# Kernel tuning notes

Measured on AMD Instinct MI355X. Metric: run time of the kernel, lower is better.

Reference implementation:

```python
import jax, jax.numpy as jnp
import numpy as np

D = 64      # hidden_dim
IN = 32     # input_dim
OUT = 8     # output_dim
WID = 128   # mlp width
B = 128     # batch
N = 16      # seq len
NS = 4      # fixed Tsit5 substeps per observation interval (stand-in for diffrax adaptive solve, max_steps=10)
EPS = 1e-8

# Tsit5 Butcher tableau
_AT = (
    (0.161,),
    (-0.008480655492356989, 0.335480655492357),
    (2.8971530571054935, -6.359448489975075, 4.3622954328695815),
    (5.325864828439257, -11.748883564062828, 7.4955393428898365, -0.09249506636175525),
    (5.86145544294642, -12.92096931784711, 8.159367898576159, -0.071584973281401, -0.028269050394068383),
)
_CT = (0.0, 0.161, 0.327, 0.9, 0.9800255409045097, 1.0)
_BT = (0.09646076681806523, 0.01, 0.4798896504144996, 1.379008574103742, -3.290069515436081, 2.324710524099774)


def _mlp(params, x, act):
    for (Wl, bl) in params[:-1]:
        x = act(Wl @ x + bl)
    Wl, bl = params[-1]
    return Wl @ x + bl


def _attn(h):
    hn = h / (jnp.linalg.norm(h) + EPS)
    return jnp.outer(hn, hn).reshape(-1)


def _field(t, h, a, fp, gp, sf, sg):
    Am = jax.nn.softmax(a.reshape(D, D), axis=-1)
    hp = Am @ h  # h @ softmax(A).T
    inp = jnp.concatenate([hp, t.reshape(1)])
    h_dot = sf * jnp.tanh(_mlp(fp, inp, jax.nn.silu))
    a_dot = sg * jnp.tanh(_mlp(gp, inp, jax.nn.silu))
    return h_dot, a_dot


def setup_inputs() -> dict:
    key = jax.random.key(0)
    ks = jax.random.split(key, 24)
    lin = lambda k, o, i: (jax.random.normal(k, (o, i), jnp.float32) / np.sqrt(i)).astype(jnp.float32)
    dt = jax.random.uniform(ks[0], (B, N), minval=0.05, maxval=0.15)
    ts = jnp.cumsum(dt, axis=1).astype(jnp.float32)
    observations = jax.random.normal(ks[1], (B, N, IN), jnp.float32)
    return {
        "ts": ts, "observations": observations,
        "f_w0": lin(ks[2], WID, D + 1), "f_b0": jnp.zeros((WID,), jnp.float32),
        "f_w1": lin(ks[3], WID, WID),   "f_b1": jnp.zeros((WID,), jnp.float32),
        "f_w2": lin(ks[4], D, WID),     "f_b2": jnp.zeros((D,), jnp.float32),
        "g_w0": lin(ks[5], WID, D + 1), "g_b0": jnp.zeros((WID,), jnp.float32),
        "g_w1": lin(ks[6], WID, WID),   "g_b1": jnp.zeros((WID,), jnp.float32),
        "g_w2": lin(ks[7], D * D, WID), "g_b2": jnp.zeros((D * D,), jnp.float32),
        "f_scale": jnp.array(1.0, jnp.float32), "g_scale": jnp.array(1.0, jnp.float32),
        "rnn_wh": lin(ks[8], D, D), "rnn_wx": lin(ks[9], D, IN), "rnn_b": jnp.zeros((D,), jnp.float32),
        "o_w0": lin(ks[10], WID, D),  "o_b0": jnp.zeros((WID,), jnp.float32),
        "o_w1": lin(ks[11], WID, WID), "o_b1": jnp.zeros((WID,), jnp.float32),
        "o_w2": lin(ks[12], OUT, WID), "o_b2": jnp.zeros((OUT,), jnp.float32),
    }


def reference(ts, observations, f_w0, f_b0, f_w1, f_b1, f_w2, f_b2,
              g_w0, g_b0, g_w1, g_b1, g_w2, g_b2, f_scale, g_scale,
              rnn_wh, rnn_wx, rnn_b, o_w0, o_b0, o_w1, o_b1, o_w2, o_b2):
    fp = ((f_w0, f_b0), (f_w1, f_b1), (f_w2, f_b2))
    gp = ((g_w0, g_b0), (g_w1, g_b1), (g_w2, g_b2))
    op = ((o_w0, o_b0), (o_w1, o_b1), (o_w2, o_b2))

    def single(ts1, obs1):
        h0 = jnp.tanh(rnn_wx @ obs1[0] + rnn_b)  # hidden_linear(zeros) == 0
        a0 = _attn(h0)

        def step(carry, inp):
            h, a = carry
            t0, t1, x = inp
            dt = (t1 - t0) / NS

            def sub(c, i):
                hh, aa = c
                t = t0 + i * dt
                k1h, k1a = _field(t, hh, aa, fp, gp, f_scale, g_scale)
                kh, ka = [k1h], [k1a]
                for s in range(5):
                    hs = hh + dt * sum(_AT[s][j] * kh[j] for j in range(s + 1))
                    as_ = aa + dt * sum(_AT[s][j] * ka[j] for j in range(s + 1))
                    kdh, kda = _field(t + _CT[s + 1] * dt, hs, as_, fp, gp, f_scale, g_scale)
                    kh.append(kdh); ka.append(kda)
                hn = hh + dt * sum(_BT[j] * kh[j] for j in range(6))
                an = aa + dt * sum(_BT[j] * ka[j] for j in range(6))
                return (hn, an), None

            (h_prime, _), _ = jax.lax.scan(sub, (h, a), jnp.arange(NS, dtype=ts1.dtype))
            h_new = jnp.tanh(rnn_wh @ h_prime + rnn_wx @ x + rnn_b)
            return (h_new, _attn(h_new)), None

        (hf, _), _ = jax.lax.scan(step, (h0, a0), (ts1[:-1], ts1[1:], obs1[1:]))
        return _mlp(op, hf, jnp.tanh)

    return jax.vmap(single)(ts, observations)  # (B, OUT), matches batched_call
```

## Files before the change

kernel.cpp:

```cpp
#include <hip/hip_runtime.h>
#include <hip/hip_bf16.h>

#define DH    64
#define INW   32
#define OUTW  8
#define WIDW  128
#define BATCH 128
#define SEQN  16
#define NSUB  4
#define NT    1024

#define OFF_G8   0
#define OFF_L0F  131072
#define OFF_L0G  135296
#define OFF_L1F  139520
#define OFF_L1G  147712
#define OFF_FH   155904
#define OFF_RWH  160000
#define OFF_RWX  164096
#define OFF_OW0  166144
#define OFF_OW1  174336
#define OFF_OW2  190720
#define WS_TOT   191744

typedef float f32x2 __attribute__((ext_vector_type(2)));

__device__ __forceinline__ float fast_tanh(float x){
  float ax = fabsf(x);
  float e  = __expf(-2.f*ax);
  float r  = __fdividef(1.f - e, 1.f + e);
  return copysignf(r, x);
}
__device__ __forceinline__ float fast_silu(float x){
  return x * __fdividef(1.f, 1.f + __expf(-x));
}
__device__ __forceinline__ uint32_t f2bf(float x){
  uint32_t u = __float_as_uint(x);
  return (u + 0x7fffu + ((u >> 16) & 1u)) >> 16;
}
__device__ __forceinline__ uint32_t f32_to_e4m3fn(float x){
  uint32_t u = __float_as_uint(x);
  uint32_t s = (u >> 31) << 7;
  float ax = fabsf(x);
  uint32_t code;
  if (ax < 0.015625f){
    int m = (int)rintf(ax * 512.0f);
    code = s | (uint32_t)m;
  } else {
    uint32_t bb = (u & 0x7FFFFFFFu) + 0x7FFFFu + ((u >> 20) & 1u);
    uint32_t E  = (bb >> 23) - 120u;
    uint32_t mag = (E << 3) | ((bb >> 20) & 7u);
    if (mag > 0x7Eu) mag = 0x7Eu;
    code = s | mag;
  }
  return code;
}

#if __has_builtin(__builtin_amdgcn_cvt_pk_f32_fp8)
__device__ __forceinline__ f32x2 fp8_lo(uint32_t u){ return __builtin_amdgcn_cvt_pk_f32_fp8(u, false); }
__device__ __forceinline__ f32x2 fp8_hi(uint32_t u){ return __builtin_amdgcn_cvt_pk_f32_fp8(u, true); }
#else
__device__ __forceinline__ float fp8_dec1(uint32_t v){
  uint32_t em = v & 0x7Fu;
  float mag;
  if (em >= 8u) mag = __uint_as_float((em + 960u) << 20);
  else          mag = (float)em * 0.001953125f;
  return (v & 0x80u) ? -mag : mag;
}
__device__ __forceinline__ f32x2 fp8_lo(uint32_t u){ f32x2 r; r[0]=fp8_dec1(u&0xFFu); r[1]=fp8_dec1((u>>8)&0xFFu); return r; }
__device__ __forceinline__ f32x2 fp8_hi(uint32_t u){ f32x2 r; r[0]=fp8_dec1((u>>16)&0xFFu); r[1]=fp8_dec1((u>>24)&0xFFu); return r; }
#endif

__device__ __forceinline__ float bflo(uint32_t u){ return __uint_as_float(u << 16); }
__device__ __forceinline__ float bfhi(uint32_t u){ return __uint_as_float(u & 0xFFFF0000u); }

__global__ void prep(const float* __restrict__ fw0, const float* __restrict__ fw1,
                     const float* __restrict__ fw2, const float* __restrict__ gw0,
                     const float* __restrict__ gw1, const float* __restrict__ gw2,
                     const float* __restrict__ rwh, const float* __restrict__ rwx,
                     const float* __restrict__ ow0, const float* __restrict__ ow1,
                     const float* __restrict__ ow2, uint32_t* __restrict__ wsu)
{
  int i = blockIdx.x * 256 + threadIdx.x;
  if (i >= WS_TOT) return;
  float* wsf = (float*)wsu;
  if (i < OFF_L0F){
    int k4 = i >> 12, e = i & 4095;
    uint32_t u = 0;
    #pragma unroll
    for (int j = 0; j < 4; ++j) u |= f32_to_e4m3fn(gw2[e*128 + 4*k4 + j]) << (8*j);
    wsu[i] = u;
  }
  else if (i < OFF_L0G){ int j=i-OFF_L0F; int k2=j>>7, o=j&127; int k0=2*k2;
    uint32_t lo = f2bf(fw0[o*65+k0]); uint32_t hi = (k0+1<65)? f2bf(fw0[o*65+k0+1]) : 0u;
    wsu[i] = lo | (hi<<16); }
  else if (i < OFF_L1F){ int j=i-OFF_L0G; int k2=j>>7, o=j&127; int k0=2*k2;
    uint32_t lo = f2bf(gw0[o*65+k0]); uint32_t hi = (k0+1<65)? f2bf(gw0[o*65+k0+1]) : 0u;
    wsu[i] = lo | (hi<<16); }
  else if (i < OFF_L1G){ int j=i-OFF_L1F; int k2=j>>7, o=j&127;
    wsu[i] = f2bf(fw1[o*128+2*k2]) | (f2bf(fw1[o*128+2*k2+1])<<16); }
  else if (i < OFF_FH){ int j=i-OFF_L1G; int k2=j>>7, o=j&127;
    wsu[i] = f2bf(gw1[o*128+2*k2]) | (f2bf(gw1[o*128+2*k2+1])<<16); }
  else if (i < OFF_RWH){ int j=i-OFF_FH; int k2=j>>6, o=j&63;
    wsu[i] = f2bf(fw2[o*128+2*k2]) | (f2bf(fw2[o*128+2*k2+1])<<16); }
  else if (i < OFF_RWX){ int j=i-OFF_RWH; int k=j>>6, o=j&63; wsf[i] = rwh[o*64+k]; }
  else if (i < OFF_OW0){ int j=i-OFF_RWX; int k=j>>6, o=j&63; wsf[i] = rwx[o*32+k]; }
  else if (i < OFF_OW1){ int j=i-OFF_OW0; int k=j>>7, o=j&127; wsf[i] = ow0[o*64+k]; }
  else if (i < OFF_OW2){ int j=i-OFF_OW1; int k=j>>7, o=j&127; wsf[i] = ow1[o*128+k]; }
  else                 { int j=i-OFF_OW2; int k=j>>3, o=j&7;  wsf[i] = ow2[o*128+k]; }
}

__global__ __launch_bounds__(NT, 4) void ace_main(
    const float* __restrict__ ts,
    const float* __restrict__ obs,
    const float* __restrict__ fb0, const float* __restrict__ fb1, const float* __restrict__ fb2,
    const float* __restrict__ gb0, const float* __restrict__ gb1, const float* __restrict__ gb2,
    const float* __restrict__ fsc, const float* __restrict__ gsc,
    const float* __restrict__ rnnb,
    const float* __restrict__ ob0, const float* __restrict__ ob1, const float* __restrict__ ob2,
    uint32_t* __restrict__ wsu,
    float* __restrict__ outp)
{
  constexpr float ATc[5][5] = {
    {0.161f, 0.f, 0.f, 0.f, 0.f},
    {-0.008480655492356989f, 0.335480655492357f, 0.f, 0.f, 0.f},
    {2.8971530571054935f, -6.359448489975075f, 4.3622954328695815f, 0.f, 0.f},
    {5.325864828439257f, -11.748883564062828f, 7.4955393428898365f, -0.09249506636175525f, 0.f},
    {5.86145544294642f, -12.92096931784711f, 8.159367898576159f, -0.071584973281401f, -0.028269050394068383f}};
  constexpr float CTc[6] = {0.f, 0.161f, 0.327f, 0.9f, 0.9800255409045097f, 1.f};
  constexpr float BTc[6] = {0.09646076681806523f, 0.01f, 0.4798896504144996f,
                            1.379008574103742f, -3.290069515436081f, 2.324710524099774f};

  const int tid = threadIdx.x;
  const int b   = blockIdx.x;
  const float* wsf = (const float*)wsu;

  const int row = tid >> 4;
  const int c4  = tid & 15;
  const int e0  = 4*tid;

  __shared__ uint32_t sL0f[33*129], sL0g[33*129];
  __shared__ uint32_t sL1f[64*129], sL1g[64*129];
  __shared__ uint32_t sFH[64*65];
  __shared__ __align__(16) float h_st[DH], h_b[DH];
  __shared__ __align__(16) float inp[72];
  __shared__ __align__(16) float zf0[WIDW], zg0[WIDW], zf1[WIDW], zg1[WIDW];
  __shared__ float sFB0[WIDW], sGB0[WIDW], sFB1[WIDW], sGB1[WIDW], sFB2[DH];
  __shared__ float red;

  for (int i = tid; i < 33*128; i += NT){
    int k2 = i >> 7, o = i & 127; int d = k2*129 + o;
    sL0f[d] = wsu[OFF_L0F + i]; sL0g[d] = wsu[OFF_L0G + i];
  }
  for (int i = tid; i < 64*128; i += NT){
    int k2 = i >> 7, o = i & 127; int d = k2*129 + o;
    sL1f[d] = wsu[OFF_L1F + i]; sL1g[d] = wsu[OFF_L1G + i];
  }
  for (int i = tid; i < 64*64; i += NT){
    int k2 = i >> 6, o = i & 63;
    sFH[k2*65 + o] = wsu[OFF_FH + i];
  }
  if (tid < WIDW){ sFB0[tid]=fb0[tid]; sGB0[tid]=gb0[tid]; sFB1[tid]=fb1[tid]; sGB1[tid]=gb1[tid]; }
  if (tid < DH) sFB2[tid] = fb2[tid];

  const uint32_t* g8 = wsu + OFF_G8;
  const float4 gb2v = *(const float4*)&gb2[e0];
  const float sf = fsc[0], sg = gsc[0];

  float a_b[4];
  float ka[6][4];
  float khr[6];

  auto attn_from_h = [&](){
    __syncthreads();
    if (tid < DH){
      float v = h_b[tid]; v = v*v;
      #pragma unroll
      for (int off = 32; off > 0; off >>= 1) v += __shfl_xor(v, off, 64);
      if (tid == 0) red = __fdividef(1.f, sqrtf(v) + 1e-8f);
      h_st[tid] = h_b[tid];
    }
    __syncthreads();
    const float inv = red;
    const float hr = h_b[row] * inv;
    const float4 hc = *(const float4*)&h_b[4*c4];
    a_b[0] = hr * (hc.x * inv);
    a_b[1] = hr * (hc.y * inv);
    a_b[2] = hr * (hc.z * inv);
    a_b[3] = hr * (hc.w * inv);
  };

  auto field_eval = [&](int si, float dtn, float t, const float (&a_s)[4], float (&ka_out)[4]){
    {
      float m = fmaxf(fmaxf(a_s[0], a_s[1]), fmaxf(a_s[2], a_s[3]));
      m = fmaxf(m, __shfl_xor(m, 1, 64));
      m = fmaxf(m, __shfl_xor(m, 2, 64));
      m = fmaxf(m, __shfl_xor(m, 4, 64));
      m = fmaxf(m, __shfl_xor(m, 8, 64));
      const float4 hv = *(const float4*)&h_st[4*c4];
      float e0v = __expf(a_s[0]-m), e1v = __expf(a_s[1]-m);
      float e2v = __expf(a_s[2]-m), e3v = __expf(a_s[3]-m);
      float es = (e0v+e1v) + (e2v+e3v);
      float hs = fmaf(e0v,hv.x, fmaf(e1v,hv.y, fmaf(e2v,hv.z, e3v*hv.w)));
      es += __shfl_xor(es, 1, 64); hs += __shfl_xor(hs, 1, 64);
      es += __shfl_xor(es, 2, 64); hs += __shfl_xor(hs, 2, 64);
      es += __shfl_xor(es, 4, 64); hs += __shfl_xor(hs, 4, 64);
      es += __shfl_xor(es, 8, 64); hs += __shfl_xor(hs, 8, 64);
      if (c4 == 0) inp[row] = __fdividef(hs, es);
      if (tid == 0) inp[DH] = t;
    }
    __syncthreads();
    {
      const bool isf = tid < 512;
      const uint32_t* wL0 = isf ? sL0f : sL0g;
      const int o = (tid >> 2) & 127, p = tid & 3;
      float acc = 0.f;
      #pragma unroll
      for (int j = 0; j < 8; ++j){
        const int k2 = p*8 + j;
        const uint32_t u = wL0[k2*129 + o];
        const f32x2 z = *(const f32x2*)&inp[2*k2];
        acc = fmaf(bflo(u), z[0], acc);
        acc = fmaf(bfhi(u), z[1], acc);
      }
      if (p == 0) acc = fmaf(bflo(wL0[32*129 + o]), inp[64], acc);
      acc += __shfl_xor(acc, 1, 64);
      acc += __shfl_xor(acc, 2, 64);
      if (p == 0) (isf ? zf0 : zg0)[o] = fast_silu(acc + (isf ? sFB0 : sGB0)[o]);
    }
    __syncthreads();
    {
      const bool isf = tid < 512;
      const uint32_t* wL1 = isf ? sL1f : sL1g;
      const float* zi = isf ? zf0 : zg0;
      const int o = (tid >> 2) & 127, p = tid & 3;
      float acc = 0.f;
      #pragma unroll
      for (int j = 0; j < 16; ++j){
        const int k2 = p*16 + j;
        const uint32_t u = wL1[k2*129 + o];
        const f32x2 z = *(const f32x2*)&zi[2*k2];
        acc = fmaf(bflo(u), z[0], acc);
        acc = fmaf(bfhi(u), z[1], acc);
      }
      acc += __shfl_xor(acc, 1, 64);
      acc += __shfl_xor(acc, 2, 64);
      if (p == 0) (isf ? zf1 : zg1)[o] = fast_silu(acc + (isf ? sFB1 : sGB1)[o]);
    }
    __syncthreads();
    if (tid < 512){
      const int o = tid >> 3, p = tid & 7;
      float acc = 0.f;
      #pragma unroll
      for (int j = 0; j < 8; ++j){
        const int k2 = p*8 + j;
        const uint32_t u = sFH[k2*65 + o];
        const f32x2 z = *(const f32x2*)&zf1[2*k2];
        acc = fmaf(bflo(u), z[0], acc);
        acc = fmaf(bfhi(u), z[1], acc);
      }
      acc += __shfl_xor(acc, 1, 64);
      acc += __shfl_xor(acc, 2, 64);
      acc += __shfl_xor(acc, 4, 64);
      if (p == 0){
        khr[si] = sf * fast_tanh(acc + sFB2[o]);
        if (si < 5){
          float s = 0.f;
          #pragma unroll
          for (int j = 0; j <= si; ++j) s = fmaf(ATc[si][j], khr[j], s);
          h_st[o] = fmaf(dtn, s, h_b[o]);
        } else {
          float s = 0.f;
          #pragma unroll
          for (int j = 0; j < 6; ++j) s = fmaf(BTc[j], khr[j], s);
          const float hn = fmaf(dtn, s, h_b[o]);
          h_b[o] = hn;
          h_st[o] = hn;
        }
      }
    }
    {
      f32x2 ac0 = {0.f,0.f}, ac1 = {0.f,0.f}, ac2 = {0.f,0.f}, ac3 = {0.f,0.f};
      #pragma unroll 8
      for (int k4 = 0; k4 < 32; ++k4){
        const uint4 w = *(const uint4*)(g8 + k4*4096 + e0);
        const float4 zz = *(const float4*)&zg1[4*k4];
        const f32x2 z01 = {zz.x, zz.y}, z23 = {zz.z, zz.w};
        ac0 = fp8_lo(w.x)*z01 + ac0;  ac0 = fp8_hi(w.x)*z23 + ac0;
        ac1 = fp8_lo(w.y)*z01 + ac1;  ac1 = fp8_hi(w.y)*z23 + ac1;
        ac2 = fp8_lo(w.z)*z01 + ac2;  ac2 = fp8_hi(w.z)*z23 + ac2;
        ac3 = fp8_lo(w.w)*z01 + ac3;  ac3 = fp8_hi(w.w)*z23 + ac3;
      }
      ka_out[0] = sg * fast_tanh(ac0[0] + ac0[1] + gb2v.x);
      ka_out[1] = sg * fast_tanh(ac1[0] + ac1[1] + gb2v.y);
      ka_out[2] = sg * fast_tanh(ac2[0] + ac2[1] + gb2v.z);
      ka_out[3] = sg * fast_tanh(ac3[0] + ac3[1] + gb2v.w);
    }
    __syncthreads();
  };

  if (tid < DH){
    float acc = rnnb[tid];
    const float* x0 = obs + b*(SEQN*INW);
    #pragma unroll
    for (int k = 0; k < INW; ++k) acc = fmaf(wsf[OFF_RWX + k*64 + tid], x0[k], acc);
    h_b[tid] = fast_tanh(acc);
  }
  attn_from_h();

  for (int n = 0; n < SEQN-1; ++n){
    const float t0  = ts[b*SEQN + n];
    const float t1  = ts[b*SEQN + n + 1];
    const float dtn = (t1 - t0) * 0.25f;

    for (int isub = 0; isub < NSUB; ++isub){
      const float tb = fmaf((float)isub, dtn, t0);
      field_eval(0, dtn, tb, a_b, ka[0]);

      #pragma unroll
      for (int s = 0; s < 5; ++s){
        float a_s[4];
        #pragma unroll
        for (int i = 0; i < 4; ++i){
          float acc = 0.f;
          #pragma unroll
          for (int j = 0; j <= s; ++j) acc = fmaf(ATc[s][j], ka[j][i], acc);
          a_s[i] = fmaf(dtn, acc, a_b[i]);
        }
        field_eval(s+1, dtn, fmaf(CTc[s+1], dtn, tb), a_s, ka[s+1]);
      }

      #pragma unroll
      for (int i = 0; i < 4; ++i){
        float acc = 0.f;
        #pragma unroll
        for (int j = 0; j < 6; ++j) acc = fmaf(BTc[j], ka[j][i], acc);
        a_b[i] = fmaf(dtn, acc, a_b[i]);
      }
    }

    float hnew = 0.f;
    if (tid < DH){
      float acc = rnnb[tid];
      const float* x = obs + (b*SEQN + (n+1))*INW;
      #pragma unroll
      for (int k = 0; k < INW; ++k) acc = fmaf(wsf[OFF_RWX + k*64 + tid], x[k], acc);
      #pragma unroll 8
      for (int k = 0; k < DH; ++k)  acc = fmaf(wsf[OFF_RWH + k*64 + tid], h_b[k], acc);
      hnew = fast_tanh(acc);
    }
    __syncthreads();
    if (tid < DH) h_b[tid] = hnew;
    attn_from_h();
  }

  __syncthreads();
  if (tid < WIDW){
    float acc = ob0[tid];
    #pragma unroll 8
    for (int k = 0; k < DH; ++k) acc = fmaf(wsf[OFF_OW0 + k*128 + tid], h_b[k], acc);
    zf0[tid] = fast_tanh(acc);
  }
  __syncthreads();
  if (tid < WIDW){
    float acc = ob1[tid];
    #pragma unroll 8
    for (int k = 0; k < WIDW; ++k) acc = fmaf(wsf[OFF_OW1 + k*128 + tid], zf0[k], acc);
    zf1[tid] = fast_tanh(acc);
  }
  __syncthreads();
  if (tid < OUTW){
    float acc = ob2[tid];
    #pragma unroll 8
    for (int k = 0; k < WIDW; ++k) acc = fmaf(wsf[OFF_OW2 + k*8 + tid], zf1[k], acc);
    outp[b*OUTW + tid] = acc;
  }
}

extern "C" void kernel_launch(void* const* d_in, const int* in_sizes, int n_in,
                              void* d_out, int out_size, void* d_ws, size_t ws_size,
                              hipStream_t stream)
{
  const float* ts   = (const float*)d_in[0];
  const float* obs  = (const float*)d_in[1];
  const float* fw0  = (const float*)d_in[2];
  const float* fb0  = (const float*)d_in[3];
  const float* fw1  = (const float*)d_in[4];
  const float* fb1  = (const float*)d_in[5];
  const float* fw2  = (const float*)d_in[6];
  const float* fb2  = (const float*)d_in[7];
  const float* gw0  = (const float*)d_in[8];
  const float* gb0  = (const float*)d_in[9];
  const float* gw1  = (const float*)d_in[10];
  const float* gb1  = (const float*)d_in[11];
  const float* gw2  = (const float*)d_in[12];
  const float* gb2  = (const float*)d_in[13];
  const float* fsc  = (const float*)d_in[14];
  const float* gsc  = (const float*)d_in[15];
  const float* rwh  = (const float*)d_in[16];
  const float* rwx  = (const float*)d_in[17];
  const float* rnb  = (const float*)d_in[18];
  const float* ow0  = (const float*)d_in[19];
  const float* ob0  = (const float*)d_in[20];
  const float* ow1  = (const float*)d_in[21];
  const float* ob1  = (const float*)d_in[22];
  const float* ow2  = (const float*)d_in[23];
  const float* ob2  = (const float*)d_in[24];
  uint32_t* wsu = (uint32_t*)d_ws;
  float* outp = (float*)d_out;

  prep<<<(WS_TOT + 255)/256, 256, 0, stream>>>(
      fw0, fw1, fw2, gw0, gw1, gw2, rwh, rwx, ow0, ow1, ow2, wsu);
  ace_main<<<BATCH, NT, 0, stream>>>(
      ts, obs, fb0, fb1, fb2, gb0, gb1, gb2, fsc, gsc, rnb, ob0, ob1, ob2, wsu, outp);
}
```

Baseline: 3.524 ms.

## Process two batch elements per block to share streamed g-layer weights

New measurement: 5.257 ms. 49.2% more time.

```diff
diff --git a/kernel.cpp b/kernel.cpp
--- a/kernel.cpp
+++ b/kernel.cpp
@@ -132,9 +132,12 @@
                             1.379008574103742f, -3.290069515436081f, 2.324710524099774f};
 
   const int tid = threadIdx.x;
-  const int b   = blockIdx.x;
+  const int b0  = blockIdx.x * 2;
+  const int b1  = b0 + 1;
   const float* wsf = (const float*)wsu;
 
+  const int bt  = tid >> 9;
+  const int st  = tid & 511;
   const int row = tid >> 4;
   const int c4  = tid & 15;
   const int e0  = 4*tid;
@@ -142,11 +145,11 @@
   __shared__ uint32_t sL0f[33*129], sL0g[33*129];
   __shared__ uint32_t sL1f[64*129], sL1g[64*129];
   __shared__ uint32_t sFH[64*65];
-  __shared__ __align__(16) float h_st[DH], h_b[DH];
-  __shared__ __align__(16) float inp[72];
-  __shared__ __align__(16) float zf0[WIDW], zg0[WIDW], zf1[WIDW], zg1[WIDW];
+  __shared__ __align__(16) float h_st[2][DH], h_b[2][DH];
+  __shared__ __align__(16) float inp[2][72];
+  __shared__ __align__(16) float zf0[2][WIDW], zg0[2][WIDW], zf1[2][WIDW], zg1[2][WIDW];
   __shared__ float sFB0[WIDW], sGB0[WIDW], sFB1[WIDW], sGB1[WIDW], sFB2[DH];
-  __shared__ float red;
+  __shared__ float red[2];
 
   for (int i = tid; i < 33*128; i += NT){
     int k2 = i >> 7, o = i & 127; int d = k2*129 + o;
@@ -167,213 +170,261 @@
   const float4 gb2v = *(const float4*)&gb2[e0];
   const float sf = fsc[0], sg = gsc[0];
 
-  float a_b[4];
-  float ka[6][4];
+  float a_b[2][4];
+  float ka[6][2][4];
   float khr[6];
 
   auto attn_from_h = [&](){
     __syncthreads();
-    if (tid < DH){
-      float v = h_b[tid]; v = v*v;
+    if (tid < 2*DH){
+      const int bb = tid >> 6, o = tid & 63;
+      float v = h_b[bb][o]; v = v*v;
       #pragma unroll
       for (int off = 32; off > 0; off >>= 1) v += __shfl_xor(v, off, 64);
-      if (tid == 0) red = __fdividef(1.f, sqrtf(v) + 1e-8f);
-      h_st[tid] = h_b[tid];
-    }
-    __syncthreads();
-    const float inv = red;
-    const float hr = h_b[row] * inv;
-    const float4 hc = *(const float4*)&h_b[4*c4];
-    a_b[0] = hr * (hc.x * inv);
-    a_b[1] = hr * (hc.y * inv);
-    a_b[2] = hr * (hc.z * inv);
-    a_b[3] = hr * (hc.w * inv);
+      if (o == 0) red[bb] = __fdividef(1.f, sqrtf(v) + 1e-8f);
+      h_st[bb][o] = h_b[bb][o];
+    }
+    __syncthreads();
+    #pragma unroll
+    for (int q = 0; q < 2; ++q){
+      const float inv = red[q];
+      const float hr = h_b[q][row] * inv;
+      const float4 hc = *(const float4*)&h_b[q][4*c4];
+      a_b[q][0] = hr * (hc.x * inv);
+      a_b[q][1] = hr * (hc.y * inv);
+      a_b[q][2] = hr * (hc.z * inv);
+      a_b[q][3] = hr * (hc.w * inv);
+    }
   };
 
-  auto field_eval = [&](int si, float dtn, float t, const float (&a_s)[4], float (&ka_out)[4]){
+  auto field_eval = [&](int si, float dtn0, float dtn1, float t0v, float t1v,
+                        const float (&a_s)[2][4], float (&ka_out)[2][4]){
     {
-      float m = fmaxf(fmaxf(a_s[0], a_s[1]), fmaxf(a_s[2], a_s[3]));
-      m = fmaxf(m, __shfl_xor(m, 1, 64));
-      m = fmaxf(m, __shfl_xor(m, 2, 64));
-      m = fmaxf(m, __shfl_xor(m, 4, 64));
-      m = fmaxf(m, __shfl_xor(m, 8, 64));
-      const float4 hv = *(const float4*)&h_st[4*c4];
-      float e0v = __expf(a_s[0]-m), e1v = __expf(a_s[1]-m);
-      float e2v = __expf(a_s[2]-m), e3v = __expf(a_s[3]-m);
-      float es = (e0v+e1v) + (e2v+e3v);
-      float hs = fmaf(e0v,hv.x, fmaf(e1v,hv.y, fmaf(e2v,hv.z, e3v*hv.w)));
-      es += __shfl_xor(es, 1, 64); hs += __shfl_xor(hs, 1, 64);
-      es += __shfl_xor(es, 2, 64); hs += __shfl_xor(hs, 2, 64);
-      es += __shfl_xor(es, 4, 64); hs += __shfl_xor(hs, 4, 64);
-      es += __shfl_xor(es, 8, 64); hs += __shfl_xor(hs, 8, 64);
-      if (c4 == 0) inp[row] = __fdividef(hs, es);
-      if (tid == 0) inp[DH] = t;
+      float m0 = fmaxf(fmaxf(a_s[0][0], a_s[0][1]), fmaxf(a_s[0][2], a_s[0][3]));
+      float m1 = fmaxf(fmaxf(a_s[1][0], a_s[1][1]), fmaxf(a_s[1][2], a_s[1][3]));
+      #pragma unroll
+      for (int off = 1; off <= 8; off <<= 1){
+        m0 = fmaxf(m0, __shfl_xor(m0, off, 64));
+        m1 = fmaxf(m1, __shfl_xor(m1, off, 64));
+      }
+      const float4 hv0 = *(const float4*)&h_st[0][4*c4];
+      const float4 hv1 = *(const float4*)&h_st[1][4*c4];
+      float ea0 = __expf(a_s[0][0]-m0), ea1 = __expf(a_s[0][1]-m0);
+      float ea2 = __expf(a_s[0][2]-m0), ea3 = __expf(a_s[0][3]-m0);
+      float eb0 = __expf(a_s[1][0]-m1), eb1 = __expf(a_s[1][1]-m1);
+      float eb2 = __expf(a_s[1][2]-m1), eb3 = __expf(a_s[1][3]-m1);
+      float es0 = (ea0+ea1)+(ea2+ea3);
+      float hs0 = fmaf(ea0,hv0.x, fmaf(ea1,hv0.y, fmaf(ea2,hv0.z, ea3*hv0.w)));
+      float es1 = (eb0+eb1)+(eb2+eb3);
+      float hs1 = fmaf(eb0,hv1.x, fmaf(eb1,hv1.y, fmaf(eb2,hv1.z, eb3*hv1.w)));
+      #pragma unroll
+      for (int off = 1; off <= 8; off <<= 1){
+        es0 += __shfl_xor(es0, off, 64); hs0 += __shfl_xor(hs0, off, 64);
+        es1 += __shfl_xor(es1, off, 64); hs1 += __shfl_xor(hs1, off, 64);
+      }
+      if (c4 == 0){
+        inp[0][row] = __fdividef(hs0, es0);
+        inp[1][row] = __fdividef(hs1, es1);
+      }
+      if (tid == 0){ inp[0][DH] = t0v; inp[1][DH] = t1v; }
     }
     __syncthreads();
     {
-      const bool isf = tid < 512;
+      const bool isf = st < 256;
       const uint32_t* wL0 = isf ? sL0f : sL0g;
-      const int o = (tid >> 2) & 127, p = tid & 3;
+      const int o = (st >> 1) & 127, p = st & 1;
+      const float* ib = inp[bt];
       float acc = 0.f;
       #pragma unroll
-      for (int j = 0; j < 8; ++j){
-        const int k2 = p*8 + j;
+      for (int j = 0; j < 16; ++j){
+        const int k2 = p*16 + j;
         const uint32_t u = wL0[k2*129 + o];
-        const f32x2 z = *(const f32x2*)&inp[2*k2];
+        const f32x2 z = *(const f32x2*)&ib[2*k2];
         acc = fmaf(bflo(u), z[0], acc);
         acc = fmaf(bfhi(u), z[1], acc);
       }
-      if (p == 0) acc = fmaf(bflo(wL0[32*129 + o]), inp[64], acc);
+      if (p == 0) acc = fmaf(bflo(wL0[32*129 + o]), ib[64], acc);
       acc += __shfl_xor(acc, 1, 64);
-      acc += __shfl_xor(acc, 2, 64);
-      if (p == 0) (isf ? zf0 : zg0)[o] = fast_silu(acc + (isf ? sFB0 : sGB0)[o]);
+      if (p == 0) (isf ? zf0 : zg0)[bt][o] = fast_silu(acc + (isf ? sFB0 : sGB0)[o]);
     }
     __syncthreads();
     {
-      const bool isf = tid < 512;
+      const bool isf = st < 256;
       const uint32_t* wL1 = isf ? sL1f : sL1g;
-      const float* zi = isf ? zf0 : zg0;
-      const int o = (tid >> 2) & 127, p = tid & 3;
+      const float* zi = (isf ? zf0 : zg0)[bt];
+      const int o = (st >> 1) & 127, p = st & 1;
       float acc = 0.f;
       #pragma unroll
-      for (int j = 0; j < 16; ++j){
-        const int k2 = p*16 + j;
+      for (int j = 0; j < 32; ++j){
+        const int k2 = p*32 + j;
         const uint32_t u = wL1[k2*129 + o];
         const f32x2 z = *(const f32x2*)&zi[2*k2];
         acc = fmaf(bflo(u), z[0], acc);
         acc = fmaf(bfhi(u), z[1], acc);
       }
       acc += __shfl_xor(acc, 1, 64);
-      acc += __shfl_xor(acc, 2, 64);
-      if (p == 0) (isf ? zf1 : zg1)[o] = fast_silu(acc + (isf ? sFB1 : sGB1)[o]);
-    }
-    __syncthreads();
-    if (tid < 512){
-      const int o = tid >> 3, p = tid & 7;
+      if (p == 0) (isf ? zf1 : zg1)[bt][o] = fast_silu(acc + (isf ? sFB1 : sGB1)[o]);
+    }
+    __syncthreads();
+    if (st < 256){
+      const int o = st >> 2, p = st & 3;
+      const float* zi = zf1[bt];
       float acc = 0.f;
       #pragma unroll
-      for (int j = 0; j < 8; ++j){
-        const int k2 = p*8 + j;
+      for (int j = 0; j < 16; ++j){
+        const int k2 = p*16 + j;
         const uint32_t u = sFH[k2*65 + o];
-        const f32x2 z = *(const f32x2*)&zf1[2*k2];
+        const f32x2 z = *(const f32x2*)&zi[2*k2];
         acc = fmaf(bflo(u), z[0], acc);
         acc = fmaf(bfhi(u), z[1], acc);
       }
       acc += __shfl_xor(acc, 1, 64);
       acc += __shfl_xor(acc, 2, 64);
-      acc += __shfl_xor(acc, 4, 64);
       if (p == 0){
+        const float dtn = bt ? dtn1 : dtn0;
         khr[si] = sf * fast_tanh(acc + sFB2[o]);
         if (si < 5){
           float s = 0.f;
           #pragma unroll
           for (int j = 0; j <= si; ++j) s = fmaf(ATc[si][j], khr[j], s);
-          h_st[o] = fmaf(dtn, s, h_b[o]);
+          h_st[bt][o] = fmaf(dtn, s, h_b[bt][o]);
         } else {
           float s = 0.f;
           #pragma unroll
           for (int j = 0; j < 6; ++j) s = fmaf(BTc[j], khr[j], s);
-          const float hn = fmaf(dtn, s, h_b[o]);
-          h_b[o] = hn;
-          h_st[o] = hn;
+          const float hn = fmaf(dtn, s, h_b[bt][o]);
+          h_b[bt][o] = hn;
+          h_st[bt][o] = hn;
         }
       }
     }
     {
-      f32x2 ac0 = {0.f,0.f}, ac1 = {0.f,0.f}, ac2 = {0.f,0.f}, ac3 = {0.f,0.f};
+      f32x2 a00={0.f,0.f}, a01={0.f,0.f}, a02={0.f,0.f}, a03={0.f,0.f};
+      f32x2 a10={0.f,0.f}, a11={0.f,0.f}, a12={0.f,0.f}, a13={0.f,0.f};
       #pragma unroll 8
       for (int k4 = 0; k4 < 32; ++k4){
         const uint4 w = *(const uint4*)(g8 + k4*4096 + e0);
-        const float4 zz = *(const float4*)&zg1[4*k4];
-        const f32x2 z01 = {zz.x, zz.y}, z23 = {zz.z, zz.w};
-        ac0 = fp8_lo(w.x)*z01 + ac0;  ac0 = fp8_hi(w.x)*z23 + ac0;
-        ac1 = fp8_lo(w.y)*z01 + ac1;  ac1 = fp8_hi(w.y)*z23 + ac1;
-        ac2 = fp8_lo(w.z)*z01 + ac2;  ac2 = fp8_hi(w.z)*z23 + ac2;
-        ac3 = fp8_lo(w.w)*z01 + ac3;  ac3 = fp8_hi(w.w)*z23 + ac3;
-      }
-      ka_out[0] = sg * fast_tanh(ac0[0] + ac0[1] + gb2v.x);
-      ka_out[1] = sg * fast_tanh(ac1[0] + ac1[1] + gb2v.y);
-      ka_out[2] = sg * fast_tanh(ac2[0] + ac2[1] + gb2v.z);
-      ka_out[3] = sg * fast_tanh(ac3[0] + ac3[1] + gb2v.w);
+        const float4 za = *(const float4*)&zg1[0][4*k4];
+        const float4 zb = *(const float4*)&zg1[1][4*k4];
+        const f32x2 za01 = {za.x, za.y}, za23 = {za.z, za.w};
+        const f32x2 zb01 = {zb.x, zb.y}, zb23 = {zb.z, zb.w};
+        { const f32x2 l = fp8_lo(w.x), h = fp8_hi(w.x);
+          a00 = l*za01 + a00; a00 = h*za23 + a00;
+          a10 = l*zb01 + a10; a10 = h*zb23 + a10; }
+        { const f32x2 l = fp8_lo(w.y), h = fp8_hi(w.y);
+          a01 = l*za01 + a01; a01 = h*za23 + a01;
+          a11 = l*zb01 + a11; a11 = h*zb23 + a11; }
+        { const f32x2 l = fp8_lo(w.z), h = fp8_hi(w.z);
+          a02 = l*za01 + a02; a02 = h*za23 + a02;
+          a12 = l*zb01 + a12; a12 = h*zb23 + a12; }
+        { const f32x2 l = fp8_lo(w.w), h = fp8_hi(w.w);
+          a03 = l*za01 + a03; a03 = h*za23 + a03;
+          a13 = l*zb01 + a13; a13 = h*zb23 + a13; }
+      }
+      ka_out[0][0] = sg * fast_tanh(a00[0] + a00[1] + gb2v.x);
+      ka_out[0][1] = sg * fast_tanh(a01[0] + a01[1] + gb2v.y);
+      ka_out[0][2] = sg * fast_tanh(a02[0] + a02[1] + gb2v.z);
+      ka_out[0][3] = sg * fast_tanh(a03[0] + a03[1] + gb2v.w);
+      ka_out[1][0] = sg * fast_tanh(a10[0] + a10[1] + gb2v.x);
+      ka_out[1][1] = sg * fast_tanh(a11[0] + a11[1] + gb2v.y);
+      ka_out[1][2] = sg * fast_tanh(a12[0] + a12[1] + gb2v.z);
+      ka_out[1][3] = sg * fast_tanh(a13[0] + a13[1] + gb2v.w);
     }
     __syncthreads();
   };
 
-  if (tid < DH){
-    float acc = rnnb[tid];
-    const float* x0 = obs + b*(SEQN*INW);
+  if (tid < 2*DH){
+    const int bb = tid >> 6, o = tid & 63;
+    float acc = rnnb[o];
+    const float* x0 = obs + (bb ? b1 : b0)*(SEQN*INW);
     #pragma unroll
-    for (int k = 0; k < INW; ++k) acc = fmaf(wsf[OFF_RWX + k*64 + tid], x0[k], acc);
-    h_b[tid] = fast_tanh(acc);
+    for (int k = 0; k < INW; ++k) acc = fmaf(wsf[OFF_RWX + k*64 + o], x0[k], acc);
+    h_b[bb][o] = fast_tanh(acc);
   }
   attn_from_h();
 
   for (int n = 0; n < SEQN-1; ++n){
-    const float t0  = ts[b*SEQN + n];
-    const float t1  = ts[b*SEQN + n + 1];
-    const float dtn = (t1 - t0) * 0.25f;
+    const float t00 = ts[b0*SEQN + n], t01 = ts[b0*SEQN + n + 1];
+    const float t10 = ts[b1*SEQN + n], t11 = ts[b1*SEQN + n + 1];
+    const float dtn0 = (t01 - t00) * 0.25f;
+    const float dtn1 = (t11 - t10) * 0.25f;
 
     for (int isub = 0; isub < NSUB; ++isub){
-      const float tb = fmaf((float)isub, dtn, t0);
-      field_eval(0, dtn, tb, a_b, ka[0]);
+      const float tb0 = fmaf((float)isub, dtn0, t00);
+      const float tb1 = fmaf((float)isub, dtn1, t10);
+      field_eval(0, dtn0, dtn1, tb0, tb1, a_b, ka[0]);
 
       #pragma unroll
       for (int s = 0; s < 5; ++s){
-        float a_s[4];
+        float a_s[2][4];
+        #pragma unroll
+        for (int q = 0; q < 2; ++q){
+          const float dtn = q ? dtn1 : dtn0;
+          #pragma unroll
+          for (int i = 0; i < 4; ++i){
+            float acc = 0.f;
+            #pragma unroll
+            for (int j = 0; j <= s; ++j) acc = fmaf(ATc[s][j], ka[j][q][i], acc);
+            a_s[q][i] = fmaf(dtn, acc, a_b[q][i]);
+          }
+        }
+        field_eval(s+1, dtn0, dtn1,
+                   fmaf(CTc[s+1], dtn0, tb0), fmaf(CTc[s+1], dtn1, tb1),
+                   a_s, ka[s+1]);
+      }
+
+      #pragma unroll
+      for (int q = 0; q < 2; ++q){
+        const float dtn = q ? dtn1 : dtn0;
         #pragma unroll
         for (int i = 0; i < 4; ++i){
           float acc = 0.f;
           #pragma unroll
-          for (int j = 0; j <= s; ++j) acc = fmaf(ATc[s][j], ka[j][i], acc);
-          a_s[i] = fmaf(dtn, acc, a_b[i]);
+          for (int j = 0; j < 6; ++j) acc = fmaf(BTc[j], ka[j][q][i], acc);
+          a_b[q][i] = fmaf(dtn, acc, a_b[q][i]);
         }
-        field_eval(s+1, dtn, fmaf(CTc[s+1], dtn, tb), a_s, ka[s+1]);
-      }
-
-      #pragma unroll
-      for (int i = 0; i < 4; ++i){
-        float acc = 0.f;
-        #pragma unroll
-        for (int j = 0; j < 6; ++j) acc = fmaf(BTc[j], ka[j][i], acc);
-        a_b[i] = fmaf(dtn, acc, a_b[i]);
       }
     }
 
     float hnew = 0.f;
-    if (tid < DH){
-      float acc = rnnb[tid];
-      const float* x = obs + (b*SEQN + (n+1))*INW;
-      #pragma unroll
-      for (int k = 0; k < INW; ++k) acc = fmaf(wsf[OFF_RWX + k*64 + tid], x[k], acc);
+    if (tid < 2*DH){
+      const int bb = tid >> 6, o = tid & 63;
+      float acc = rnnb[o];
+      const float* x = obs + ((bb ? b1 : b0)*SEQN + (n+1))*INW;
+      #pragma unroll
+      for (int k = 0; k < INW; ++k) acc = fmaf(wsf[OFF_RWX + k*64 + o], x[k], acc);
       #pragma unroll 8
-      for (int k = 0; k < DH; ++k)  acc = fmaf(wsf[OFF_RWH + k*64 + tid], h_b[k], acc);
+      for (int k = 0; k < DH; ++k)  acc = fmaf(wsf[OFF_RWH + k*64 + o], h_b[bb][k], acc);
       hnew = fast_tanh(acc);
     }
     __syncthreads();
-    if (tid < DH) h_b[tid] = hnew;
+    if (tid < 2*DH){
+      const int bb = tid >> 6, o = tid & 63;
+      h_b[bb][o] = hnew;
+    }
     attn_from_h();
   }
 
   __syncthreads();
-  if (tid < WIDW){
-    float acc = ob0[tid];
+  if (st < WIDW){
+    float acc = ob0[st];
     #pragma unroll 8
-    for (int k = 0; k < DH; ++k) acc = fmaf(wsf[OFF_OW0 + k*128 + tid], h_b[k], acc);
-    zf0[tid] = fast_tanh(acc);
+    for (int k = 0; k < DH; ++k) acc = fmaf(wsf[OFF_OW0 + k*128 + st], h_b[bt][k], acc);
+    zf0[bt][st] = fast_tanh(acc);
   }
   __syncthreads();
-  if (tid < WIDW){
-    float acc = ob1[tid];
+  if (st < WIDW){
+    float acc = ob1[st];
     #pragma unroll 8
-    for (int k = 0; k < WIDW; ++k) acc = fmaf(wsf[OFF_OW1 + k*128 + tid], zf0[k], acc);
-    zf1[tid] = fast_tanh(acc);
+    for (int k = 0; k < WIDW; ++k) acc = fmaf(wsf[OFF_OW1 + k*128 + st], zf0[bt][k], acc);
+    zf1[bt][st] = fast_tanh(acc);
   }
   __syncthreads();
-  if (tid < OUTW){
-    float acc = ob2[tid];
+  if (st < OUTW){
+    float acc = ob2[st];
     #pragma unroll 8
-    for (int k = 0; k < WIDW; ++k) acc = fmaf(wsf[OFF_OW2 + k*8 + tid], zf1[k], acc);
-    outp[b*OUTW + tid] = acc;
+    for (int k = 0; k < WIDW; ++k) acc = fmaf(wsf[OFF_OW2 + k*8 + st], zf1[bt][k], acc);
+    outp[(bt ? b1 : b0)*OUTW + st] = acc;
   }
 }
 
@@ -411,6 +462,6 @@
 
   prep<<<(WS_TOT + 255)/256, 256, 0, stream>>>(
       fw0, fw1, fw2, gw0, gw1, gw2, rwh, rwx, ow0, ow1, ow2, wsu);
-  ace_main<<<BATCH, NT, 0, stream>>>(
+  ace_main<<<BATCH/2, NT, 0, stream>>>(
       ts, obs, fb0, fb1, fb2, gb0, gb1, gb2, fsc, gsc, rnb, ob0, ob1, ob2, wsu, outp);
 }
```

## Split each batch element across two cooperating blocks with global-memory flag sync

Applied to the files above, without the earlier changes.

Measured after the change: 4.289 ms. 1.22x slower.

```diff
diff --git a/kernel.cpp b/kernel.cpp
--- a/kernel.cpp
+++ b/kernel.cpp
@@ -21,7 +21,9 @@
 #define OFF_OW0  166144
 #define OFF_OW1  174336
 #define OFF_OW2  190720
-#define WS_TOT   191744
+#define OFF_HP   191744
+#define OFF_FLG  208128
+#define WS_TOT   208384
 
 typedef float f32x2 __attribute__((ext_vector_type(2)));
 
@@ -107,7 +109,9 @@
   else if (i < OFF_OW0){ int j=i-OFF_RWX; int k=j>>6, o=j&63; wsf[i] = rwx[o*32+k]; }
   else if (i < OFF_OW1){ int j=i-OFF_OW0; int k=j>>7, o=j&127; wsf[i] = ow0[o*64+k]; }
   else if (i < OFF_OW2){ int j=i-OFF_OW1; int k=j>>7, o=j&127; wsf[i] = ow1[o*128+k]; }
-  else                 { int j=i-OFF_OW2; int k=j>>3, o=j&7;  wsf[i] = ow2[o*128+k]; }
+  else if (i < OFF_HP) { int j=i-OFF_OW2; int k=j>>3, o=j&7;  wsf[i] = ow2[o*128+k]; }
+  else if (i < OFF_FLG){ wsf[i] = 0.f; }
+  else                 { wsu[i] = 0u; }
 }
 
 __global__ __launch_bounds__(NT, 4) void ace_main(
@@ -132,12 +136,15 @@
                             1.379008574103742f, -3.290069515436081f, 2.324710524099774f};
 
   const int tid = threadIdx.x;
-  const int b   = blockIdx.x;
+  const int bi  = blockIdx.x;
+  const int b   = bi & 127;
+  const int hb  = bi >> 7;
   const float* wsf = (const float*)wsu;
 
-  const int row = tid >> 4;
-  const int c4  = tid & 15;
-  const int e0  = 4*tid;
+  const int lr   = tid >> 5;
+  const int grow = hb*32 + lr;
+  const int cc   = tid & 31;
+  const int e0g  = hb*2048 + 2*tid;
 
   __shared__ uint32_t sL0f[33*129], sL0g[33*129];
   __shared__ uint32_t sL1f[64*129], sL1g[64*129];
@@ -164,12 +171,16 @@
   if (tid < DH) sFB2[tid] = fb2[tid];
 
   const uint32_t* g8 = wsu + OFF_G8;
-  const float4 gb2v = *(const float4*)&gb2[e0];
+  const float gbias0 = gb2[e0g], gbias1 = gb2[e0g + 1];
   const float sf = fsc[0], sg = gsc[0];
 
-  float a_b[4];
-  float ka[6][4];
+  float a_b[2];
+  float ka[6][2];
   float khr[6];
+  uint32_t ev = 0;
+
+  float* hp_base = (float*)(wsu + OFF_HP) + b*128;
+  uint32_t* flg  = wsu + OFF_FLG + b*2;
 
   auto attn_from_h = [&](){
     __syncthreads();
@@ -182,32 +193,43 @@
     }
     __syncthreads();
     const float inv = red;
-    const float hr = h_b[row] * inv;
-    const float4 hc = *(const float4*)&h_b[4*c4];
+    const float hr = h_b[grow] * inv;
+    const float2 hc = *(const float2*)&h_b[2*cc];
     a_b[0] = hr * (hc.x * inv);
     a_b[1] = hr * (hc.y * inv);
-    a_b[2] = hr * (hc.z * inv);
-    a_b[3] = hr * (hc.w * inv);
   };
 
-  auto field_eval = [&](int si, float dtn, float t, const float (&a_s)[4], float (&ka_out)[4]){
+  auto field_eval = [&](int si, float dtn, float t, const float (&a_s)[2], float (&ka_out)[2]){
     {
-      float m = fmaxf(fmaxf(a_s[0], a_s[1]), fmaxf(a_s[2], a_s[3]));
-      m = fmaxf(m, __shfl_xor(m, 1, 64));
-      m = fmaxf(m, __shfl_xor(m, 2, 64));
-      m = fmaxf(m, __shfl_xor(m, 4, 64));
-      m = fmaxf(m, __shfl_xor(m, 8, 64));
-      const float4 hv = *(const float4*)&h_st[4*c4];
+      float m = fmaxf(a_s[0], a_s[1]);
+      #pragma unroll
+      for (int off = 1; off <= 16; off <<= 1) m = fmaxf(m, __shfl_xor(m, off, 64));
+      const float2 hv = *(const float2*)&h_st[2*cc];
       float e0v = __expf(a_s[0]-m), e1v = __expf(a_s[1]-m);
-      float e2v = __expf(a_s[2]-m), e3v = __expf(a_s[3]-m);
-      float es = (e0v+e1v) + (e2v+e3v);
-      float hs = fmaf(e0v,hv.x, fmaf(e1v,hv.y, fmaf(e2v,hv.z, e3v*hv.w)));
-      es += __shfl_xor(es, 1, 64); hs += __shfl_xor(hs, 1, 64);
-      es += __shfl_xor(es, 2, 64); hs += __shfl_xor(hs, 2, 64);
-      es += __shfl_xor(es, 4, 64); hs += __shfl_xor(hs, 4, 64);
-      es += __shfl_xor(es, 8, 64); hs += __shfl_xor(hs, 8, 64);
-      if (c4 == 0) inp[row] = __fdividef(hs, es);
+      float es = e0v + e1v;
+      float hs = fmaf(e0v, hv.x, e1v*hv.y);
+      #pragma unroll
+      for (int off = 1; off <= 16; off <<= 1){
+        es += __shfl_xor(es, off, 64);
+        hs += __shfl_xor(hs, off, 64);
+      }
+      if (cc == 0){
+        float ip = __fdividef(hs, es);
+        inp[grow] = ip;
+        __hip_atomic_store(hp_base + (ev & 1)*64 + grow, ip,
+                           __ATOMIC_RELAXED, __HIP_MEMORY_SCOPE_AGENT);
+      }
       if (tid == 0) inp[DH] = t;
+    }
+    __syncthreads();
+    if (tid == 0)
+      __hip_atomic_store(&flg[hb], ev, __ATOMIC_RELEASE, __HIP_MEMORY_SCOPE_AGENT);
+    if (tid < 32){
+      while (__hip_atomic_load(&flg[1-hb], __ATOMIC_ACQUIRE, __HIP_MEMORY_SCOPE_AGENT) < ev)
+        __builtin_amdgcn_s_sleep(1);
+      float v = __hip_atomic_load(hp_base + (ev & 1)*64 + (1-hb)*32 + tid,
+                                  __ATOMIC_RELAXED, __HIP_MEMORY_SCOPE_AGENT);
+      inp[(1-hb)*32 + tid] = v;
     }
     __syncthreads();
     {
@@ -280,21 +302,17 @@
       }
     }
     {
-      f32x2 ac0 = {0.f,0.f}, ac1 = {0.f,0.f}, ac2 = {0.f,0.f}, ac3 = {0.f,0.f};
+      f32x2 ac0 = {0.f,0.f}, ac1 = {0.f,0.f};
       #pragma unroll 8
       for (int k4 = 0; k4 < 32; ++k4){
-        const uint4 w = *(const uint4*)(g8 + k4*4096 + e0);
+        const uint2 w = *(const uint2*)(g8 + k4*4096 + e0g);
         const float4 zz = *(const float4*)&zg1[4*k4];
         const f32x2 z01 = {zz.x, zz.y}, z23 = {zz.z, zz.w};
         ac0 = fp8_lo(w.x)*z01 + ac0;  ac0 = fp8_hi(w.x)*z23 + ac0;
         ac1 = fp8_lo(w.y)*z01 + ac1;  ac1 = fp8_hi(w.y)*z23 + ac1;
-        ac2 = fp8_lo(w.z)*z01 + ac2;  ac2 = fp8_hi(w.z)*z23 + ac2;
-        ac3 = fp8_lo(w.w)*z01 + ac3;  ac3 = fp8_hi(w.w)*z23 + ac3;
-      }
-      ka_out[0] = sg * fast_tanh(ac0[0] + ac0[1] + gb2v.x);
-      ka_out[1] = sg * fast_tanh(ac1[0] + ac1[1] + gb2v.y);
-      ka_out[2] = sg * fast_tanh(ac2[0] + ac2[1] + gb2v.z);
-      ka_out[3] = sg * fast_tanh(ac3[0] + ac3[1] + gb2v.w);
+      }
+      ka_out[0] = sg * fast_tanh(ac0[0] + ac0[1] + gbias0);
+      ka_out[1] = sg * fast_tanh(ac1[0] + ac1[1] + gbias1);
     }
     __syncthreads();
   };
@@ -315,23 +333,25 @@
 
     for (int isub = 0; isub < NSUB; ++isub){
       const float tb = fmaf((float)isub, dtn, t0);
+      ++ev;
       field_eval(0, dtn, tb, a_b, ka[0]);
 
       #pragma unroll
       for (int s = 0; s < 5; ++s){
-        float a_s[4];
+        float a_s[2];
         #pragma unroll
-        for (int i = 0; i < 4; ++i){
+        for (int i = 0; i < 2; ++i){
           float acc = 0.f;
           #pragma unroll
           for (int j = 0; j <= s; ++j) acc = fmaf(ATc[s][j], ka[j][i], acc);
           a_s[i] = fmaf(dtn, acc, a_b[i]);
         }
+        ++ev;
         field_eval(s+1, dtn, fmaf(CTc[s+1], dtn, tb), a_s, ka[s+1]);
       }
 
       #pragma unroll
-      for (int i = 0; i < 4; ++i){
+      for (int i = 0; i < 2; ++i){
         float acc = 0.f;
         #pragma unroll
         for (int j = 0; j < 6; ++j) acc = fmaf(BTc[j], ka[j][i], acc);
@@ -354,26 +374,28 @@
     attn_from_h();
   }
 
-  __syncthreads();
-  if (tid < WIDW){
-    float acc = ob0[tid];
-    #pragma unroll 8
-    for (int k = 0; k < DH; ++k) acc = fmaf(wsf[OFF_OW0 + k*128 + tid], h_b[k], acc);
-    zf0[tid] = fast_tanh(acc);
-  }
-  __syncthreads();
-  if (tid < WIDW){
-    float acc = ob1[tid];
-    #pragma unroll 8
-    for (int k = 0; k < WIDW; ++k) acc = fmaf(wsf[OFF_OW1 + k*128 + tid], zf0[k], acc);
-    zf1[tid] = fast_tanh(acc);
-  }
-  __syncthreads();
-  if (tid < OUTW){
-    float acc = ob2[tid];
-    #pragma unroll 8
-    for (int k = 0; k < WIDW; ++k) acc = fmaf(wsf[OFF_OW2 + k*8 + tid], zf1[k], acc);
-    outp[b*OUTW + tid] = acc;
+  if (hb == 0){
+    __syncthreads();
+    if (tid < WIDW){
+      float acc = ob0[tid];
+      #pragma unroll 8
+      for (int k = 0; k < DH; ++k) acc = fmaf(wsf[OFF_OW0 + k*128 + tid], h_b[k], acc);
+      zf0[tid] = fast_tanh(acc);
+    }
+    __syncthreads();
+    if (tid < WIDW){
+      float acc = ob1[tid];
+      #pragma unroll 8
+      for (int k = 0; k < WIDW; ++k) acc = fmaf(wsf[OFF_OW1 + k*128 + tid], zf0[k], acc);
+      zf1[tid] = fast_tanh(acc);
+    }
+    __syncthreads();
+    if (tid < OUTW){
+      float acc = ob2[tid];
+      #pragma unroll 8
+      for (int k = 0; k < WIDW; ++k) acc = fmaf(wsf[OFF_OW2 + k*8 + tid], zf1[k], acc);
+      outp[b*OUTW + tid] = acc;
+    }
   }
 }
 
@@ -411,6 +433,6 @@
 
   prep<<<(WS_TOT + 255)/256, 256, 0, stream>>>(
       fw0, fw1, fw2, gw0, gw1, gw2, rwh, rwx, ow0, ow1, ow2, wsu);
-  ace_main<<<BATCH, NT, 0, stream>>>(
+  ace_main<<<2*BATCH, NT, 0, stream>>>(
       ts, obs, fb0, fb1, fb2, gb0, gb1, gb2, fsc, gsc, rnb, ob0, ob1, ob2, wsu, outp);
 }
```
